# Optimization experiments

Hardware: AMD Instinct MI355X
Metric: run time of the kernel (lower is better)

The kernel has to match this reference:

```python
import jax, jax.numpy as jnp
import numpy as np

B, N, M, D = 8, 512, 64, 128
H = 64  # mlp_hidden_dim


def setup_inputs() -> dict:
    key = jax.random.key(0)
    ks = jax.random.split(key, 10)
    op_emb = jax.random.normal(ks[0], (B, N, D), dtype=jnp.float32)
    machine_emb = jax.random.normal(ks[1], (B, M, D), dtype=jnp.float32)
    edge_emb = jax.random.normal(ks[2], (B, N, M, D), dtype=jnp.float32)
    action_mask = jax.random.randint(ks[3], (B, N, M), 0, 2) > 0
    s1 = 1.0 / np.sqrt(3 * D)
    s2 = 1.0 / np.sqrt(H)
    W1 = jax.random.uniform(ks[4], (3 * D, H), jnp.float32, -s1, s1)
    b1 = jax.random.uniform(ks[5], (H,), jnp.float32, -s1, s1)
    W2 = jax.random.uniform(ks[6], (H, H), jnp.float32, -s2, s2)
    b2 = jax.random.uniform(ks[7], (H,), jnp.float32, -s2, s2)
    W3 = jax.random.uniform(ks[8], (H, 1), jnp.float32, -s2, s2)
    b3 = jax.random.uniform(ks[9], (1,), jnp.float32, -s2, s2)
    return {"op_emb": op_emb, "machine_emb": machine_emb, "edge_emb": edge_emb,
            "action_mask": action_mask,
            "W1": W1, "b1": b1, "W2": W2, "b2": b2, "W3": W3, "b3": b3}


def reference(op_emb, machine_emb, edge_emb, action_mask, W1, b1, W2, b2, W3, b3):
    # Split first linear over the three concat chunks to avoid materializing
    # the (B,N,M,3D) concat tensor (same math as cat -> Linear).
    Wo, Wm, We = W1[:D], W1[D:2 * D], W1[2 * D:]
    h = (jnp.einsum('bnd,dh->bnh', op_emb, Wo)[:, :, None, :]
         + jnp.einsum('bmd,dh->bmh', machine_emb, Wm)[:, None, :, :]
         + jnp.einsum('bnmd,dh->bnmh', edge_emb, We) + b1)  # (B,N,M,H)
    h = jax.nn.relu(h)
    h = jax.nn.relu(h @ W2 + b2)
    scores = (h @ W3 + b3)[..., 0]  # (B,N,M)
    scores = jnp.where(action_mask, scores, -jnp.inf)
    return jax.nn.log_softmax(scores.reshape(B, N * M), axis=-1)
```

## Files before the change

kernel.cpp:

```cpp
#include <hip/hip_runtime.h>
#include <math.h>

#define Bb 8
#define Nn 512
#define Mm 64
#define Dd 128
#define Hh 64
#define Gg 16
#define NEG_BIG (-1.0e30f)

typedef __bf16 bf16x8 __attribute__((ext_vector_type(8)));
typedef float  f32x4  __attribute__((ext_vector_type(4)));

#define WS_WEB   0u
#define WS_W2B   16384u
#define WS_CWSF  24576u
#define WS_AOP   155648u
#define WS_SCORE 1204224u
#define WS_PART  2252800u

#define GLOAD_LDS(gp, lp) __builtin_amdgcn_global_load_lds( \
    (const __attribute__((address_space(1))) void*)(gp),    \
    (__attribute__((address_space(3))) void*)(lp), 16, 0, 0)

__global__ __launch_bounds__(256) void prep_kernel(
    const float* __restrict__ W1, const float* __restrict__ W2,
    const float* __restrict__ op_emb, const float* __restrict__ machine_emb,
    const float* __restrict__ b1, char* __restrict__ ws)
{
    if (blockIdx.x < 48) {
        __bf16* WeB = (__bf16*)(ws + WS_WEB);
        __bf16* W2B = (__bf16*)(ws + WS_W2B);
        int idx = blockIdx.x * 256 + threadIdx.x;
        if (idx < 8192) {
            int fid = idx >> 9, rem = idx & 511;
            int lane = rem >> 3, j = rem & 7;
            int t = fid >> 2, ks = fid & 3;
            int q = lane >> 4, ln = lane & 15;
            int d = ks * 32 + q * 8 + j;
            int h = t * 16 + ln;
            WeB[idx] = (__bf16)W1[(size_t)(2 * Dd + d) * Hh + h];
        } else {
            int i2 = idx - 8192;
            int fid = i2 >> 9, rem = i2 & 511;
            int lane = rem >> 3, j = rem & 7;
            int t = fid >> 1, ks = fid & 1;
            int q = lane >> 4, ln = lane & 15;
            int k = ks * 32 + q * 8 + j;
            int h = t * 16 + ln;
            W2B[i2] = (__bf16)W2[(size_t)k * Hh + h];
        }
        return;
    }
    float* CwsF = (float*)(ws + WS_CWSF);
    float* Aop  = (float*)(ws + WS_AOP);
    const int bid = (blockIdx.x - 48) * 4 + (threadIdx.x >> 6);
    const int h = threadIdx.x & 63;
    if (bid < Bb * Mm) {
        const float* mg = machine_emb + (size_t)bid * Dd;
        const float* Wm = W1 + (size_t)Dd * Hh;
        float acc = b1[h];
#pragma unroll 8
        for (int d = 0; d < Dd; ++d) acc = fmaf(mg[d], Wm[d * Hh + h], acc);
        int b = bid >> 6, m = bid & 63;
        int wq = m >> 4, q = (m >> 2) & 3, r = m & 3;
        int t = h >> 4, ln = h & 15;
        CwsF[((((b * 4 + wq) * 4 + t) * 64) + (q * 16 + ln)) * 4 + r] = acc;
    } else {
        const int bn = bid - Bb * Mm;
        const float* og = op_emb + (size_t)bn * Dd;
        float acc = 0.f;
#pragma unroll 8
        for (int d = 0; d < Dd; ++d) acc = fmaf(og[d], W1[d * Hh + h], acc);
        Aop[(size_t)bn * Hh + h] = acc;
    }
}

__global__ __launch_bounds__(256, 1) void main_kernel(
    const float* __restrict__ edge_emb, const int* __restrict__ mask,
    const float* __restrict__ b2, const float* __restrict__ W3,
    const float* __restrict__ b3, char* __restrict__ ws)
{
    __shared__ float  sEdge[4 * 2 * 2048];
    __shared__ float  sCwsF[4096];
    __shared__ float  sAop[Gg * Hh];
    __shared__ int    sMask[Gg * Mm];
    __shared__ __bf16 sH1[Mm * 72];

    float* scores = (float*)(ws + WS_SCORE);

    const int tid  = threadIdx.x;
    const int lane = tid & 63;
    const int w    = tid >> 6;
    const int q    = lane >> 4;
    const int ln   = lane & 15;
    const int bn0  = blockIdx.x * Gg;
    const int b    = bn0 >> 9;
    const int wu   = __builtin_amdgcn_readfirstlane(w);

    const float* ebase = edge_emb + ((size_t)bn0 * Mm + w * 16 + ln) * Dd + q * 8;

    {
        float* d0 = &sEdge[(wu * 2 + 0) * 2048];
        float* d1 = &sEdge[(wu * 2 + 1) * 2048];
#pragma unroll
        for (int s = 0; s < 8; ++s)
            GLOAD_LDS(ebase + (s >> 1) * 32 + (s & 1) * 4, d0 + s * 256);
#pragma unroll
        for (int s = 0; s < 8; ++s)
            GLOAD_LDS(ebase + 8192 + (s >> 1) * 32 + (s & 1) * 4, d1 + s * 256);
    }

    {
        const f32x4* s3 = (const f32x4*)(ws + WS_CWSF) + (size_t)b * 1024;
        f32x4* d3 = (f32x4*)sCwsF;
#pragma unroll
        for (int i = 0; i < 4; ++i) d3[tid + 256 * i] = s3[tid + 256 * i];
        ((f32x4*)sAop)[tid]  = ((const f32x4*)((ws + WS_AOP)))[(size_t)bn0 * 16 + tid];
        ((int4*)sMask)[tid]  = ((const int4*)mask)[(size_t)bn0 * 16 + tid];
    }

    bf16x8 weF[16], w2F[8];
    {
        const bf16x8* WeB = (const bf16x8*)(ws + WS_WEB);
        const bf16x8* W2B = (const bf16x8*)(ws + WS_W2B);
#pragma unroll
        for (int f = 0; f < 16; ++f) weF[f] = WeB[f * 64 + lane];
#pragma unroll
        for (int f = 0; f < 8; ++f)  w2F[f] = W2B[f * 64 + lane];
    }

    float b2v[4], w3v[4];
#pragma unroll
    for (int t = 0; t < 4; ++t) { b2v[t] = b2[t * 16 + ln]; w3v[t] = W3[t * 16 + ln]; }
    const float bias3 = b3[0];

    __syncthreads();

#pragma unroll
    for (int g = 0; g < Gg; ++g) {
        const int buf = g & 1;
        const float* ldsrd = &sEdge[(wu * 2 + buf) * 2048];

        if (g == Gg - 1) __builtin_amdgcn_s_waitcnt(0x0F70);
        else             __builtin_amdgcn_s_waitcnt(0x0F78);

        f32x4 lo[4], hi[4];
#pragma unroll
        for (int ks = 0; ks < 4; ++ks) {
            lo[ks] = *(const f32x4*)&ldsrd[(ks * 2 + 0) * 256 + lane * 4];
            hi[ks] = *(const f32x4*)&ldsrd[(ks * 2 + 1) * 256 + lane * 4];
        }
        bf16x8 af[4];
#pragma unroll
        for (int ks = 0; ks < 4; ++ks) {
            bf16x8 a;
            a[0] = (__bf16)lo[ks][0]; a[1] = (__bf16)lo[ks][1];
            a[2] = (__bf16)lo[ks][2]; a[3] = (__bf16)lo[ks][3];
            a[4] = (__bf16)hi[ks][0]; a[5] = (__bf16)hi[ks][1];
            a[6] = (__bf16)hi[ks][2]; a[7] = (__bf16)hi[ks][3];
            af[ks] = a;
        }

        if (g + 2 < Gg) {
            float* dst = &sEdge[(wu * 2 + buf) * 2048];
            const float* src = ebase + (size_t)(g + 2) * 8192;
#pragma unroll
            for (int s = 0; s < 8; ++s)
                GLOAD_LDS(src + (s >> 1) * 32 + (s & 1) * 4, dst + s * 256);
        }

        f32x4 acc[4];
#pragma unroll
        for (int t = 0; t < 4; ++t) {
            f32x4 cv4 = *(const f32x4*)&sCwsF[((w * 4 + t) * 64 + lane) * 4];
            float av = sAop[g * Hh + t * 16 + ln];
            acc[t][0] = cv4[0] + av; acc[t][1] = cv4[1] + av;
            acc[t][2] = cv4[2] + av; acc[t][3] = cv4[3] + av;
        }

#pragma unroll
        for (int t = 0; t < 4; ++t)
#pragma unroll
            for (int ks = 0; ks < 4; ++ks)
                acc[t] = __builtin_amdgcn_mfma_f32_16x16x32_bf16(af[ks], weF[t * 4 + ks], acc[t], 0, 0, 0);

#pragma unroll
        for (int t = 0; t < 4; ++t)
#pragma unroll
            for (int r = 0; r < 4; ++r)
                sH1[(w * 16 + q * 4 + r) * 72 + t * 16 + ln] =
                    (__bf16)fmaxf(acc[t][r], 0.f);

        bf16x8 a2[2];
#pragma unroll
        for (int ks = 0; ks < 2; ++ks)
            a2[ks] = *(const bf16x8*)&sH1[(w * 16 + ln) * 72 + ks * 32 + q * 8];
        f32x4 c2[4];
#pragma unroll
        for (int t = 0; t < 4; ++t) c2[t] = (f32x4){0.f, 0.f, 0.f, 0.f};
#pragma unroll
        for (int t = 0; t < 4; ++t)
#pragma unroll
            for (int ks = 0; ks < 2; ++ks)
                c2[t] = __builtin_amdgcn_mfma_f32_16x16x32_bf16(a2[ks], w2F[t * 2 + ks], c2[t], 0, 0, 0);

        float p[4] = {0.f, 0.f, 0.f, 0.f};
#pragma unroll
        for (int t = 0; t < 4; ++t)
#pragma unroll
            for (int r = 0; r < 4; ++r)
                p[r] += fmaxf(c2[t][r] + b2v[t], 0.f) * w3v[t];
#pragma unroll
        for (int r = 0; r < 4; ++r) {
            p[r] += __shfl_xor(p[r], 1, 64);
            p[r] += __shfl_xor(p[r], 2, 64);
            p[r] += __shfl_xor(p[r], 4, 64);
            p[r] += __shfl_xor(p[r], 8, 64);
        }
        if (ln == 0) {
            const int m0 = w * 16 + q * 4;
            const int* mrow = &sMask[g * Mm + m0];
            float4 o;
            o.x = mrow[0] ? (p[0] + bias3) : NEG_BIG;
            o.y = mrow[1] ? (p[1] + bias3) : NEG_BIG;
            o.z = mrow[2] ? (p[2] + bias3) : NEG_BIG;
            o.w = mrow[3] ? (p[3] + bias3) : NEG_BIG;
            *(float4*)&scores[(size_t)(bn0 + g) * Mm + m0] = o;
        }
    }
}

__global__ __launch_bounds__(256) void lsm_part_kernel(char* __restrict__ ws)
{
    const float* s = (const float*)(ws + WS_SCORE);
    float* part = (float*)(ws + WS_PART);
    __shared__ float sm[4], ss[4];
    const int c = blockIdx.x;
    const int tid = threadIdx.x;
    const int lane = tid & 63, wv = tid >> 6;

    float2 v = *(const float2*)&s[(size_t)c * 512 + tid * 2];
    float m = fmaxf(v.x, v.y);
#pragma unroll
    for (int off = 1; off < 64; off <<= 1) m = fmaxf(m, __shfl_xor(m, off, 64));
    if (lane == 0) sm[wv] = m;
    __syncthreads();
    float gm = fmaxf(fmaxf(sm[0], sm[1]), fmaxf(sm[2], sm[3]));

    float e = expf(v.x - gm) + expf(v.y - gm);
#pragma unroll
    for (int off = 1; off < 64; off <<= 1) e += __shfl_xor(e, off, 64);
    if (lane == 0) ss[wv] = e;
    __syncthreads();
    if (tid == 0) {
        float2 o; o.x = gm; o.y = ss[0] + ss[1] + ss[2] + ss[3];
        *(float2*)&part[c * 2] = o;
    }
}

__global__ __launch_bounds__(256) void lsm_apply_kernel(
    const char* __restrict__ ws, float* __restrict__ out)
{
    const float4* s4 = (const float4*)(ws + WS_SCORE);
    const float* part = (const float*)(ws + WS_PART);
    __shared__ float sCC;
    const int tid = threadIdx.x;
    const int b = blockIdx.x >> 5;
    if (tid < 64) {
        float2 p = *(const float2*)&part[(b * 64 + tid) * 2];
        float gm = p.x;
#pragma unroll
        for (int off = 1; off < 64; off <<= 1) gm = fmaxf(gm, __shfl_xor(gm, off, 64));
        float l = p.y * expf(p.x - gm);
#pragma unroll
        for (int off = 1; off < 64; off <<= 1) l += __shfl_xor(l, off, 64);
        if (tid == 0) sCC = gm + logf(l);
    }
    __syncthreads();
    const float c = sCC;
    const int i = blockIdx.x * 256 + tid;
    float4 v = s4[i];
    v.x -= c; v.y -= c; v.z -= c; v.w -= c;
    ((float4*)out)[i] = v;
}

extern "C" void kernel_launch(void* const* d_in, const int* in_sizes, int n_in,
                              void* d_out, int out_size, void* d_ws, size_t ws_size,
                              hipStream_t stream)
{
    const float* op_emb      = (const float*)d_in[0];
    const float* machine_emb = (const float*)d_in[1];
    const float* edge_emb    = (const float*)d_in[2];
    const int*   mask        = (const int*)  d_in[3];
    const float* W1 = (const float*)d_in[4];
    const float* b1 = (const float*)d_in[5];
    const float* W2 = (const float*)d_in[6];
    const float* b2 = (const float*)d_in[7];
    const float* W3 = (const float*)d_in[8];
    const float* b3 = (const float*)d_in[9];
    char* ws = (char*)d_ws;

    prep_kernel<<<48 + 1152, 256, 0, stream>>>(W1, W2, op_emb, machine_emb, b1, ws);
    main_kernel<<<(Bb * Nn) / Gg, 256, 0, stream>>>(edge_emb, mask, b2, W3, b3, ws);
    lsm_part_kernel<<<512, 256, 0, stream>>>(ws);
    lsm_apply_kernel<<<256, 256, 0, stream>>>(ws, (float*)d_out);
}
```

Baseline: 233.5 us.

## Fuse softmax partial reduction into main kernel and halve rows per block

Each main_kernel block now keeps a running max and sum-of-exponentials for its masked scores and writes one (max, sum) pair per block. This replaces the separate lsm_part_kernel launch and its re-read of the score buffer. Rows per block drop from 16 to 8, which doubles the grid to 512 blocks and gives exactly 64 partials per batch. Launch bounds now allow two blocks per CU, and the per-batch machine term is held in registers instead of being staged through shared memory. In exchange the main loop gains per-element exp work that is repeated across the 16 lanes of each group, and register pressure rises.

```diff
diff --git a/kernel.cpp b/kernel.cpp
--- a/kernel.cpp
+++ b/kernel.cpp
@@ -6,7 +6,7 @@
 #define Mm 64
 #define Dd 128
 #define Hh 64
-#define Gg 16
+#define Gg 8
 #define NEG_BIG (-1.0e30f)
 
 typedef __bf16 bf16x8 __attribute__((ext_vector_type(8)));
@@ -76,18 +76,19 @@
     }
 }
 
-__global__ __launch_bounds__(256, 1) void main_kernel(
+__global__ __launch_bounds__(256, 2) void main_kernel(
     const float* __restrict__ edge_emb, const int* __restrict__ mask,
     const float* __restrict__ b2, const float* __restrict__ W3,
     const float* __restrict__ b3, char* __restrict__ ws)
 {
     __shared__ float  sEdge[4 * 2 * 2048];
-    __shared__ float  sCwsF[4096];
     __shared__ float  sAop[Gg * Hh];
     __shared__ int    sMask[Gg * Mm];
     __shared__ __bf16 sH1[Mm * 72];
+    __shared__ float  sRed[8];
 
     float* scores = (float*)(ws + WS_SCORE);
+    float* part   = (float*)(ws + WS_PART);
 
     const int tid  = threadIdx.x;
     const int lane = tid & 63;
@@ -111,16 +112,13 @@
             GLOAD_LDS(ebase + 8192 + (s >> 1) * 32 + (s & 1) * 4, d1 + s * 256);
     }
 
-    {
-        const f32x4* s3 = (const f32x4*)(ws + WS_CWSF) + (size_t)b * 1024;
-        f32x4* d3 = (f32x4*)sCwsF;
-#pragma unroll
-        for (int i = 0; i < 4; ++i) d3[tid + 256 * i] = s3[tid + 256 * i];
-        ((f32x4*)sAop)[tid]  = ((const f32x4*)((ws + WS_AOP)))[(size_t)bn0 * 16 + tid];
-        ((int4*)sMask)[tid]  = ((const int4*)mask)[(size_t)bn0 * 16 + tid];
+    if (tid < 128) {
+        ((f32x4*)sAop)[tid] = ((const f32x4*)(ws + WS_AOP))[(size_t)bn0 * 16 + tid];
+        ((int4*)sMask)[tid] = ((const int4*)mask)[(size_t)bn0 * 16 + tid];
     }
 
     bf16x8 weF[16], w2F[8];
+    f32x4  cv[4];
     {
         const bf16x8* WeB = (const bf16x8*)(ws + WS_WEB);
         const bf16x8* W2B = (const bf16x8*)(ws + WS_W2B);
@@ -128,12 +126,17 @@
         for (int f = 0; f < 16; ++f) weF[f] = WeB[f * 64 + lane];
 #pragma unroll
         for (int f = 0; f < 8; ++f)  w2F[f] = W2B[f * 64 + lane];
+        const f32x4* CwsF = (const f32x4*)(ws + WS_CWSF) + (size_t)b * 1024;
+#pragma unroll
+        for (int t = 0; t < 4; ++t)  cv[t] = CwsF[(w * 4 + t) * 64 + lane];
     }
 
     float b2v[4], w3v[4];
 #pragma unroll
     for (int t = 0; t < 4; ++t) { b2v[t] = b2[t * 16 + ln]; w3v[t] = W3[t * 16 + ln]; }
     const float bias3 = b3[0];
+
+    float m_loc = NEG_BIG, l_loc = 0.f;
 
     __syncthreads();
 
@@ -173,10 +176,9 @@
         f32x4 acc[4];
 #pragma unroll
         for (int t = 0; t < 4; ++t) {
-            f32x4 cv4 = *(const f32x4*)&sCwsF[((w * 4 + t) * 64 + lane) * 4];
             float av = sAop[g * Hh + t * 16 + ln];
-            acc[t][0] = cv4[0] + av; acc[t][1] = cv4[1] + av;
-            acc[t][2] = cv4[2] + av; acc[t][3] = cv4[3] + av;
+            acc[t][0] = cv[t][0] + av; acc[t][1] = cv[t][1] + av;
+            acc[t][2] = cv[t][2] + av; acc[t][3] = cv[t][3] + av;
         }
 
 #pragma unroll
@@ -218,44 +220,46 @@
             p[r] += __shfl_xor(p[r], 4, 64);
             p[r] += __shfl_xor(p[r], 8, 64);
         }
+        const int m0 = w * 16 + q * 4;
+        const int* mrow = &sMask[g * Mm + m0];
+        float vv[4];
+#pragma unroll
+        for (int r = 0; r < 4; ++r) {
+            float v = p[r] + bias3;
+            vv[r] = mrow[r] ? v : NEG_BIG;
+            if (mrow[r]) {
+                float mn = fmaxf(m_loc, v);
+                l_loc = l_loc * expf(m_loc - mn) + expf(v - mn);
+                m_loc = mn;
+            }
+        }
         if (ln == 0) {
-            const int m0 = w * 16 + q * 4;
-            const int* mrow = &sMask[g * Mm + m0];
-            float4 o;
-            o.x = mrow[0] ? (p[0] + bias3) : NEG_BIG;
-            o.y = mrow[1] ? (p[1] + bias3) : NEG_BIG;
-            o.z = mrow[2] ? (p[2] + bias3) : NEG_BIG;
-            o.w = mrow[3] ? (p[3] + bias3) : NEG_BIG;
+            float4 o; o.x = vv[0]; o.y = vv[1]; o.z = vv[2]; o.w = vv[3];
             *(float4*)&scores[(size_t)(bn0 + g) * Mm + m0] = o;
         }
     }
-}
-
-__global__ __launch_bounds__(256) void lsm_part_kernel(char* __restrict__ ws)
-{
-    const float* s = (const float*)(ws + WS_SCORE);
-    float* part = (float*)(ws + WS_PART);
-    __shared__ float sm[4], ss[4];
-    const int c = blockIdx.x;
-    const int tid = threadIdx.x;
-    const int lane = tid & 63, wv = tid >> 6;
-
-    float2 v = *(const float2*)&s[(size_t)c * 512 + tid * 2];
-    float m = fmaxf(v.x, v.y);
-#pragma unroll
-    for (int off = 1; off < 64; off <<= 1) m = fmaxf(m, __shfl_xor(m, off, 64));
-    if (lane == 0) sm[wv] = m;
-    __syncthreads();
-    float gm = fmaxf(fmaxf(sm[0], sm[1]), fmaxf(sm[2], sm[3]));
-
-    float e = expf(v.x - gm) + expf(v.y - gm);
-#pragma unroll
-    for (int off = 1; off < 64; off <<= 1) e += __shfl_xor(e, off, 64);
-    if (lane == 0) ss[wv] = e;
+
+#pragma unroll
+    for (int off = 16; off <= 32; off <<= 1) {
+        float mo = __shfl_xor(m_loc, off, 64);
+        float lo2 = __shfl_xor(l_loc, off, 64);
+        float mn = fmaxf(m_loc, mo);
+        l_loc = l_loc * expf(m_loc - mn) + lo2 * expf(mo - mn);
+        m_loc = mn;
+    }
+    if (lane == 0) { sRed[w * 2] = m_loc; sRed[w * 2 + 1] = l_loc; }
     __syncthreads();
     if (tid == 0) {
-        float2 o; o.x = gm; o.y = ss[0] + ss[1] + ss[2] + ss[3];
-        *(float2*)&part[c * 2] = o;
+        float gm = sRed[0], gl = sRed[1];
+#pragma unroll
+        for (int k = 1; k < 4; ++k) {
+            float mo = sRed[k * 2], lo2 = sRed[k * 2 + 1];
+            float mn = fmaxf(gm, mo);
+            gl = gl * expf(gm - mn) + lo2 * expf(mo - mn);
+            gm = mn;
+        }
+        float2 o; o.x = gm; o.y = gl;
+        *(float2*)&part[blockIdx.x * 2] = o;
     }
 }
 
@@ -303,6 +307,5 @@
 
     prep_kernel<<<48 + 1152, 256, 0, stream>>>(W1, W2, op_emb, machine_emb, b1, ws);
     main_kernel<<<(Bb * Nn) / Gg, 256, 0, stream>>>(edge_emb, mask, b2, W3, b3, ws);
-    lsm_part_kernel<<<512, 256, 0, stream>>>(ws);
     lsm_apply_kernel<<<256, 256, 0, stream>>>(ws, (float*)d_out);
 }
```

New measurement: 227.2 us. 2.7% less time.
